# Optimization experiments

Hardware: AMD Instinct MI355X
Metric: run time of the kernel (lower is better)

The kernel has to match this reference:

```python
import jax, jax.numpy as jnp
import numpy as np

N_NODES = 50000

def _add_self_loops(edge_index, n):
    loop = jnp.arange(n, dtype=edge_index.dtype)
    src = jnp.concatenate([edge_index[0], loop])
    dst = jnp.concatenate([edge_index[1], loop])
    return src, dst

def _gcn_conv(x, src, dst, W, b, n):
    h = x @ W
    deg = jax.ops.segment_sum(jnp.ones_like(dst, dtype=h.dtype), dst, num_segments=n)
    inv_sqrt = jnp.where(deg > 0, jax.lax.rsqrt(deg), 0.0)
    coef = inv_sqrt[src] * inv_sqrt[dst]            # [E]
    msg = h[src] * coef[:, None]                     # [E, hidden]
    return jax.ops.segment_sum(msg, dst, num_segments=n) + b

def _gat_conv(x, src, dst, W, att_src, att_dst, b, n, heads, out_dim):
    # PyG GATConv, concat=False -> mean over heads; self-loops already added
    h = (x @ W).reshape(n, heads, out_dim)           # [N, H, F]
    a_src = jnp.sum(h * att_src, axis=-1)            # [N, H]
    a_dst = jnp.sum(h * att_dst, axis=-1)            # [N, H]
    e = a_src[src] + a_dst[dst]                      # [E, H]
    e = jax.nn.leaky_relu(e, negative_slope=0.2)
    # neighborhood softmax over edges grouped by destination
    m = jax.ops.segment_max(e, dst, num_segments=n)  # [N, H]
    ex = jnp.exp(e - m[dst])
    denom = jax.ops.segment_sum(ex, dst, num_segments=n)
    alpha = ex / denom[dst]                          # [E, H]
    out = jax.ops.segment_sum(h[src] * alpha[:, :, None], dst, num_segments=n)  # [N, H, F]
    return out.mean(axis=1) + b                      # concat=False -> head mean

def setup_inputs() -> dict:
    key = jax.random.key(0)
    ks = jax.random.split(key, 12)
    n, input_dim, hidden, output_dim, heads = N_NODES, 128, 128, 64, 2
    gat_out = hidden // 2
    x = jax.random.normal(ks[0], (n, input_dim), dtype=jnp.float32)
    edge_index = jax.random.randint(ks[1], (2, 800000), 0, n, dtype=jnp.int64)
    s = lambda fi, fo: float(np.sqrt(1.0 / fi))
    W1 = jax.random.normal(ks[2], (input_dim, hidden), dtype=jnp.float32) * s(input_dim, hidden)
    b1 = jnp.zeros((hidden,), dtype=jnp.float32)
    Wg = jax.random.normal(ks[3], (hidden, heads * gat_out), dtype=jnp.float32) * s(hidden, gat_out)
    att_src = jax.random.normal(ks[4], (heads, gat_out), dtype=jnp.float32) * s(gat_out, 1)
    att_dst = jax.random.normal(ks[5], (heads, gat_out), dtype=jnp.float32) * s(gat_out, 1)
    bg = jnp.zeros((gat_out,), dtype=jnp.float32)
    W3 = jax.random.normal(ks[6], (gat_out, output_dim), dtype=jnp.float32) * s(gat_out, output_dim)
    b3 = jnp.zeros((output_dim,), dtype=jnp.float32)
    return {"x": x, "edge_index": edge_index, "W1": W1, "b1": b1, "Wg": Wg,
            "att_src": att_src, "att_dst": att_dst, "bg": bg, "W3": W3, "b3": b3}

def reference(x, edge_index, W1, b1, Wg, att_src, att_dst, bg, W3, b3):
    n = x.shape[0]
    heads, gat_out = att_src.shape
    src, dst = _add_self_loops(edge_index, n)
    # dropout is identity in eval mode
    h = _gcn_conv(x, src, dst, W1, b1, n)
    h = jax.nn.relu(h)
    h = _gat_conv(h, src, dst, Wg, att_src, att_dst, bg, n, heads, gat_out)
    h = jax.nn.elu(h)
    return _gcn_conv(h, src, dst, W3, b3, n)
```

## Files before the change

kernel.cpp:

```cpp
#include <hip/hip_runtime.h>
#include <hip/hip_bf16.h>
#include <math.h>

#define N_NODES 50000
#define E0      800000
#define E_TOT   (E0 + N_NODES)
#define SCAP    512

using bf16 = __hip_bfloat16;
typedef __attribute__((ext_vector_type(8))) short bfrag;
typedef __attribute__((ext_vector_type(4))) float ffrag;

static __device__ __forceinline__ float bfu2f_lo(unsigned u){ return __uint_as_float(u << 16); }
static __device__ __forceinline__ float bfu2f_hi(unsigned u){ return __uint_as_float(u & 0xffff0000u); }

static __device__ __forceinline__ unsigned packbf(float a, float b){
    bf16 x = __float2bfloat16(a), y = __float2bfloat16(b);
    unsigned short ux = *reinterpret_cast<unsigned short*>(&x);
    unsigned short uy = *reinterpret_cast<unsigned short*>(&y);
    return ((unsigned)uy << 16) | ux;
}

static __device__ __forceinline__ int detect_f32(const unsigned* xu){
    int lane = threadIdx.x & 63;
    unsigned ex = (xu[lane] >> 7) & 0xFF;
    return (__ballot(ex < 100 || ex > 140) != 0ULL);
}
static __device__ __forceinline__ int detect_i32(const int* ei){
    int lane = threadIdx.x & 63;
    return (__ballot(ei[2 * lane + 1] != 0) != 0ULL);
}

static __device__ __forceinline__ float ldany(const void* p, int i, int isf32){
    return isf32 ? ((const float*)p)[i] : __bfloat162float(((const bf16*)p)[i]);
}

__global__ void k_convert(const void* __restrict__ xv,
                          const void* W1, const void* Wg, const void* W3,
                          const void* b1, const void* bg, const void* b3,
                          const void* as_, const void* ad_,
                          bf16* __restrict__ W1p, bf16* __restrict__ Wgp,
                          bf16* __restrict__ W3p, float* __restrict__ vecf,
                          bf16* __restrict__ xb, int* __restrict__ deg){
    const int NXB = (N_NODES * 32 + 255) / 256;
    int b = blockIdx.x, t = threadIdx.x;
    if (b >= 148 + NXB){
        int i = (b - 148 - NXB) * 256 + t;
        if (i < N_NODES) deg[i] = 0;
        return;
    }
    int isf = detect_f32((const unsigned*)xv);
    if (b >= 148){
        int i = (b - 148) * 256 + t;
        if (i < N_NODES * 32){
            if (isf){
                float4 v = ((const float4*)xv)[i];
                ((uint2*)xb)[i] = make_uint2(packbf(v.x, v.y), packbf(v.z, v.w));
            } else {
                ((uint2*)xb)[i] = ((const uint2*)xv)[i];
            }
        }
        return;
    }
    if (b < 16){
        int dd = b * 256 + t;
        int j  = dd & 7;
        int L  = (dd >> 3) & 63;
        int kc = (dd >> 9) & 1;
        int ct = dd >> 10;
        int k = kc * 32 + ((L >> 4) << 3) + j;
        int n = ct * 16 + (L & 15);
        W3p[dd] = __float2bfloat16(ldany(W3, k * 64 + n, isf));
    }
    else if (b < 18){
        int i = (b - 16) * 256 + t;
        float v;
        if      (i < 128) v = ldany(b1,  i,       isf);
        else if (i < 192) v = ldany(bg,  i - 128, isf);
        else if (i < 256) v = ldany(b3,  i - 192, isf);
        else if (i < 384) v = ldany(as_, i - 256, isf);
        else              v = ldany(ad_, i - 384, isf);
        vecf[i] = v;
    } else {
        int d = (b - 18) * 256 + t;
        const void* Wsrc = (d < 16384) ? W1 : Wg;
        bf16* Wdst = (d < 16384) ? W1p : Wgp;
        int dd = d & 16383;
        int j  = dd & 7;
        int L  = (dd >> 3) & 63;
        int kc = (dd >> 9) & 3;
        int ct = dd >> 11;
        int k = kc * 32 + ((L >> 4) << 3) + j;
        int n = ct * 16 + (L & 15);
        Wdst[dd] = __float2bfloat16(ldany(Wsrc, k * 128 + n, isf));
    }
}


static __device__ __forceinline__ int load_dst(const int* ei, int e, int is32){
    if (e >= E0) return e - E0;
    return is32 ? ei[E0 + e] : (int)((const long long*)ei)[E0 + e];
}
static __device__ __forceinline__ int load_src(const int* ei, int e, int is32){
    if (e >= E0) return e - E0;
    return is32 ? ei[e] : (int)((const long long*)ei)[e];
}

__global__ void k_count(const int* __restrict__ ei, int* __restrict__ deg,
                        int* __restrict__ rank){
    int is32 = detect_i32(ei);
    int e = blockIdx.x * blockDim.x + threadIdx.x;
    if (e >= E_TOT) return;
    int dst = load_dst(ei, e, is32);
    int src = load_src(ei, e, is32);
    if ((unsigned)dst >= N_NODES || (unsigned)src >= N_NODES) return;
    rank[e] = atomicAdd(&deg[dst], 1);
}

__global__ void k_scanA(const int* __restrict__ deg, int* __restrict__ tmp, int* __restrict__ blk){
    __shared__ int s[256];
    int t = threadIdx.x;
    int i = blockIdx.x * 256 + t;
    int v = (i < N_NODES) ? deg[i] : 0;
    s[t] = v; __syncthreads();
    for (int off = 1; off < 256; off <<= 1){
        int x = (t >= off) ? s[t - off] : 0;
        __syncthreads();
        s[t] += x;
        __syncthreads();
    }
    if (t == 255) blk[blockIdx.x] = s[255];
    if (i < N_NODES) tmp[i] = s[t] - v;
}

__global__ void k_scanC(int* __restrict__ row_ptr, const int* __restrict__ blk,
                        const int* __restrict__ deg, float* __restrict__ inv_sqrt,
                        int nb){
    __shared__ int s[256];
    int t = threadIdx.x;
    int B = blockIdx.x;
    s[t] = (t < nb && t < B) ? blk[t] : 0;
    __syncthreads();
    for (int off = 128; off; off >>= 1){
        if (t < off) s[t] += s[t + off];
        __syncthreads();
    }
    int base = s[0];
    int i = B * 256 + t;
    if (i < N_NODES){
        row_ptr[i] += base;
        int d = deg[i];
        inv_sqrt[i] = (d > 0) ? rsqrtf((float)d) : 0.0f;
    }
    if (i == 0) row_ptr[N_NODES] = E_TOT;
}

__global__ void k_fill(const int* __restrict__ ei, const int* __restrict__ row_ptr,
                       const float* __restrict__ isq, const int* __restrict__ rank,
                       int2* __restrict__ ecr){
    int is32 = detect_i32(ei);
    int e = blockIdx.x * blockDim.x + threadIdx.x;
    if (e >= E_TOT) return;
    int dst = load_dst(ei, e, is32);
    int src = load_src(ei, e, is32);
    if ((unsigned)dst >= N_NODES || (unsigned)src >= N_NODES) return;
    int pos = row_ptr[dst] + rank[e];
    float c = isq[dst] * isq[src];
    ecr[pos] = make_int2(src, __float_as_int(c));
}

__global__ __launch_bounds__(256) void k_gather(
        const uint4* __restrict__ xb16, const int* __restrict__ rp,
        const int2* __restrict__ ecr, uint4* __restrict__ Xa16){
    __shared__ int   scsr[SCAP];
    __shared__ float scf[SCAP];
    int n0 = blockIdx.x * 4;
    int b0 = rp[n0];
    int stot = min(rp[n0 + 4] - b0, SCAP);
    for (int i = threadIdx.x; i < stot; i += 256){
        int2 ev = ecr[b0 + i];
        scsr[i] = ev.x;
        scf[i]  = __int_as_float(ev.y);
    }
    __syncthreads();

    int w = threadIdx.x >> 6, lane = threadIdx.x & 63;
    int q4 = lane >> 4, fz = lane & 15;
    int n = n0 + w;
    float a0=0,a1=0,a2=0,a3=0,a4=0,a5=0,a6=0,a7=0;
    int b = rp[n] - b0, e = rp[n + 1] - b0;
    int elim = min(e, stot);
    #pragma unroll 2
    for (int i = b + q4; i < elim; i += 4){
        int s = scsr[i];
        float c = scf[i];
        uint4 v = xb16[(size_t)s * 16 + fz];
        a0 += c * bfu2f_lo(v.x);  a1 += c * bfu2f_hi(v.x);
        a2 += c * bfu2f_lo(v.y);  a3 += c * bfu2f_hi(v.y);
        a4 += c * bfu2f_lo(v.z);  a5 += c * bfu2f_hi(v.z);
        a6 += c * bfu2f_lo(v.w);  a7 += c * bfu2f_hi(v.w);
    }
    int start = max(b, stot);
    int i0 = start + (((b + q4) - start) & 3);
    for (int i = i0; i < e; i += 4){
        int2 ev = ecr[b0 + i];
        float c = __int_as_float(ev.y);
        uint4 v = xb16[(size_t)ev.x * 16 + fz];
        a0 += c * bfu2f_lo(v.x);  a1 += c * bfu2f_hi(v.x);
        a2 += c * bfu2f_lo(v.y);  a3 += c * bfu2f_hi(v.y);
        a4 += c * bfu2f_lo(v.z);  a5 += c * bfu2f_hi(v.z);
        a6 += c * bfu2f_lo(v.w);  a7 += c * bfu2f_hi(v.w);
    }
    a0 += __shfl_xor(a0, 32, 64);  a0 += __shfl_xor(a0, 16, 64);
    a1 += __shfl_xor(a1, 32, 64);  a1 += __shfl_xor(a1, 16, 64);
    a2 += __shfl_xor(a2, 32, 64);  a2 += __shfl_xor(a2, 16, 64);
    a3 += __shfl_xor(a3, 32, 64);  a3 += __shfl_xor(a3, 16, 64);
    a4 += __shfl_xor(a4, 32, 64);  a4 += __shfl_xor(a4, 16, 64);
    a5 += __shfl_xor(a5, 32, 64);  a5 += __shfl_xor(a5, 16, 64);
    a6 += __shfl_xor(a6, 32, 64);  a6 += __shfl_xor(a6, 16, 64);
    a7 += __shfl_xor(a7, 32, 64);  a7 += __shfl_xor(a7, 16, 64);
    if (lane < 16){
        uint4 o;
        o.x = packbf(a0, a1);  o.y = packbf(a2, a3);
        o.z = packbf(a4, a5);  o.w = packbf(a6, a7);
        Xa16[(size_t)n * 16 + fz] = o;
    }
}

template<int EPI>
__global__ __launch_bounds__(512) void k_gemm_mfma(
        const bf16* __restrict__ A, const bf16* __restrict__ Wp,
        const float* __restrict__ vecf, bf16* __restrict__ O,
        float* __restrict__ aS, float* __restrict__ aD){
    __shared__ float sA[16][8];
    __shared__ float sD[16][8];
    int wid  = threadIdx.x >> 6;
    int lane = threadIdx.x & 63;
    int n0 = blockIdx.x * 16;
    int m = lane & 15, q = lane >> 4;

    const bfrag* Ap = (const bfrag*)(A + (size_t)(n0 + m) * 128);
    const bfrag* Bp = (const bfrag*)Wp + (size_t)wid * 256 + lane;

    ffrag c = {0.f, 0.f, 0.f, 0.f};
    #pragma unroll
    for (int kc = 0; kc < 4; ++kc){
        bfrag af = Ap[kc * 4 + q];
        bfrag bf = Bp[kc * 64];
        c = __builtin_amdgcn_mfma_f32_16x16x32_bf16(af, bf, c, 0, 0, 0);
    }
    __syncthreads();

    int col = wid * 16 + m;
    if (EPI == 0){
        float bb = vecf[col];
        #pragma unroll
        for (int r = 0; r < 4; ++r){
            int row = n0 + q * 4 + r;
            O[(size_t)row * 128 + col] = __float2bfloat16(fmaxf(c[r] + bb, 0.f));
        }
    } else {
        int f = col & 63, h = col >> 6;
        float as_v = vecf[256 + h * 64 + f];
        float ad_v = vecf[384 + h * 64 + f];
        float ps[4], pd[4];
        #pragma unroll
        for (int r = 0; r < 4; ++r){
            int row = n0 + q * 4 + r;
            O[(size_t)row * 128 + f * 2 + h] = __float2bfloat16(c[r]);
            ps[r] = c[r] * as_v;
            pd[r] = c[r] * ad_v;
        }
        #pragma unroll
        for (int off = 1; off < 16; off <<= 1){
            #pragma unroll
            for (int r = 0; r < 4; ++r){
                ps[r] += __shfl_xor(ps[r], off, 64);
                pd[r] += __shfl_xor(pd[r], off, 64);
            }
        }
        if (m == 0){
            #pragma unroll
            for (int r = 0; r < 4; ++r){
                int rl = q * 4 + r;
                sA[rl][wid] = ps[r];
                sD[rl][wid] = pd[r];
            }
        }
        __syncthreads();
        int t = threadIdx.x;
        if (t < 64){
            int rl = t >> 2, hh = (t >> 1) & 1, which = t & 1;
            const float (*S)[8] = which ? sD : sA;
            float v = S[rl][hh * 4 + 0] + S[rl][hh * 4 + 1]
                    + S[rl][hh * 4 + 2] + S[rl][hh * 4 + 3];
            float* dp = which ? aD : aS;
            dp[(size_t)(n0 + rl) * 2 + hh] = v;
        }
    }
}

__global__ __launch_bounds__(256) void k_gemm_z(
        const bf16* __restrict__ Y, const bf16* __restrict__ W3p,
        bf16* __restrict__ Z){
    int wid  = threadIdx.x >> 6;
    int lane = threadIdx.x & 63;
    int n0 = blockIdx.x * 16;
    int m = lane & 15, q = lane >> 4;

    const bfrag* Ap = (const bfrag*)(Y + (size_t)(n0 + m) * 64);
    const bfrag* Bp = (const bfrag*)W3p + (size_t)wid * 128 + lane;

    ffrag c = {0.f, 0.f, 0.f, 0.f};
    #pragma unroll
    for (int kc = 0; kc < 2; ++kc){
        bfrag af = Ap[kc * 4 + q];
        bfrag bf = Bp[kc * 64];
        c = __builtin_amdgcn_mfma_f32_16x16x32_bf16(af, bf, c, 0, 0, 0);
    }
    int col = wid * 16 + m;
    #pragma unroll
    for (int r = 0; r < 4; ++r){
        int row = n0 + q * 4 + r;
        Z[(size_t)row * 64 + col] = __float2bfloat16(c[r]);
    }
}

__global__ __launch_bounds__(256) void k_gat(
        const uint4* __restrict__ X2v, const int* __restrict__ rp,
        const int2* __restrict__ ecr, const float2* __restrict__ a_src,
        const float2* __restrict__ a_dst, const float* __restrict__ vecf,
        uint2* __restrict__ Yu2){
    __shared__ int    scsr[SCAP];
    __shared__ float2 pe[SCAP];
    int n0 = blockIdx.x * 4;
    int b0 = rp[n0];
    int stot = min(rp[n0 + 4] - b0, SCAP);
    for (int i = threadIdx.x; i < stot; i += 256) scsr[i] = ecr[b0 + i].x;
    __syncthreads();

    int w = threadIdx.x >> 6, lane = threadIdx.x & 63;
    int q4 = lane >> 4, fz = lane & 15;
    int n = n0 + w;
    float2 ad = a_dst[n];
    int b = rp[n] - b0, e = rp[n + 1] - b0;
    int elim = min(e, stot);

    for (int i = b + lane; i < elim; i += 64){
        float2 av = a_src[scsr[i]];
        float e0 = av.x + ad.x, e1 = av.y + ad.y;
        e0 = (e0 > 0.f) ? e0 : 0.2f * e0;
        e1 = (e1 > 0.f) ? e1 : 0.2f * e1;
        pe[i] = make_float2(__expf(e0), __expf(e1));
    }

    float l0 = 0.f, l1 = 0.f;
    float o00=0,o01=0, o10=0,o11=0, o20=0,o21=0, o30=0,o31=0;
    #pragma unroll 2
    for (int i = b + q4; i < elim; i += 4){
        float2 p = pe[i];
        uint4 v = X2v[(size_t)scsr[i] * 16 + fz];
        l0  += p.x;                  l1  += p.y;
        o00 += p.x * bfu2f_lo(v.x);  o01 += p.y * bfu2f_hi(v.x);
        o10 += p.x * bfu2f_lo(v.y);  o11 += p.y * bfu2f_hi(v.y);
        o20 += p.x * bfu2f_lo(v.z);  o21 += p.y * bfu2f_hi(v.z);
        o30 += p.x * bfu2f_lo(v.w);  o31 += p.y * bfu2f_hi(v.w);
    }
    int start = max(b, stot);
    int i0 = start + (((b + q4) - start) & 3);
    for (int i = i0; i < e; i += 4){
        int s = ecr[b0 + i].x;
        float2 av = a_src[s];
        uint4 v = X2v[(size_t)s * 16 + fz];
        float e0 = av.x + ad.x, e1 = av.y + ad.y;
        e0 = (e0 > 0.f) ? e0 : 0.2f * e0;
        e1 = (e1 > 0.f) ? e1 : 0.2f * e1;
        float p0 = __expf(e0), p1 = __expf(e1);
        l0  += p0;                 l1  += p1;
        o00 += p0 * bfu2f_lo(v.x); o01 += p1 * bfu2f_hi(v.x);
        o10 += p0 * bfu2f_lo(v.y); o11 += p1 * bfu2f_hi(v.y);
        o20 += p0 * bfu2f_lo(v.z); o21 += p1 * bfu2f_hi(v.z);
        o30 += p0 * bfu2f_lo(v.w); o31 += p1 * bfu2f_hi(v.w);
    }
    l0  += __shfl_xor(l0, 32, 64);   l0  += __shfl_xor(l0, 16, 64);
    l1  += __shfl_xor(l1, 32, 64);   l1  += __shfl_xor(l1, 16, 64);
    o00 += __shfl_xor(o00, 32, 64);  o00 += __shfl_xor(o00, 16, 64);
    o01 += __shfl_xor(o01, 32, 64);  o01 += __shfl_xor(o01, 16, 64);
    o10 += __shfl_xor(o10, 32, 64);  o10 += __shfl_xor(o10, 16, 64);
    o11 += __shfl_xor(o11, 32, 64);  o11 += __shfl_xor(o11, 16, 64);
    o20 += __shfl_xor(o20, 32, 64);  o20 += __shfl_xor(o20, 16, 64);
    o21 += __shfl_xor(o21, 32, 64);  o21 += __shfl_xor(o21, 16, 64);
    o30 += __shfl_xor(o30, 32, 64);  o30 += __shfl_xor(o30, 16, 64);
    o31 += __shfl_xor(o31, 32, 64);  o31 += __shfl_xor(o31, 16, 64);
    if (lane < 16){
        float v0 = 0.5f * (o00 / l0 + o01 / l1) + vecf[128 + 4 * fz + 0];
        float v1 = 0.5f * (o10 / l0 + o11 / l1) + vecf[128 + 4 * fz + 1];
        float v2 = 0.5f * (o20 / l0 + o21 / l1) + vecf[128 + 4 * fz + 2];
        float v3 = 0.5f * (o30 / l0 + o31 / l1) + vecf[128 + 4 * fz + 3];
        v0 = (v0 > 0.f) ? v0 : expm1f(v0);
        v1 = (v1 > 0.f) ? v1 : expm1f(v1);
        v2 = (v2 > 0.f) ? v2 : expm1f(v2);
        v3 = (v3 > 0.f) ? v3 : expm1f(v3);
        Yu2[(size_t)n * 16 + fz] = make_uint2(packbf(v0, v1), packbf(v2, v3));
    }
}

__global__ __launch_bounds__(256) void k_gather_out(
        const uint2* __restrict__ Zu2, const int* __restrict__ rp,
        const int2* __restrict__ ecr, const float* __restrict__ vecf,
        float4* __restrict__ out4){
    __shared__ int   scsr[SCAP];
    __shared__ float scf[SCAP];
    int n0 = blockIdx.x * 4;
    int b0 = rp[n0];
    int stot = min(rp[n0 + 4] - b0, SCAP);
    for (int i = threadIdx.x; i < stot; i += 256){
        int2 ev = ecr[b0 + i];
        scsr[i] = ev.x;
        scf[i]  = __int_as_float(ev.y);
    }
    __syncthreads();

    int w = threadIdx.x >> 6, lane = threadIdx.x & 63;
    int q4 = lane >> 4, fz = lane & 15;
    int n = n0 + w;
    float a0 = 0.f, a1 = 0.f, a2 = 0.f, a3 = 0.f;
    int b = rp[n] - b0, e = rp[n + 1] - b0;
    int elim = min(e, stot);
    #pragma unroll 2
    for (int i = b + q4; i < elim; i += 4){
        float c = scf[i];
        uint2 v = Zu2[(size_t)scsr[i] * 16 + fz];
        a0 += c * bfu2f_lo(v.x);  a1 += c * bfu2f_hi(v.x);
        a2 += c * bfu2f_lo(v.y);  a3 += c * bfu2f_hi(v.y);
    }
    int start = max(b, stot);
    int i0 = start + (((b + q4) - start) & 3);
    for (int i = i0; i < e; i += 4){
        int2 ev = ecr[b0 + i];
        float c = __int_as_float(ev.y);
        uint2 v = Zu2[(size_t)ev.x * 16 + fz];
        a0 += c * bfu2f_lo(v.x);  a1 += c * bfu2f_hi(v.x);
        a2 += c * bfu2f_lo(v.y);  a3 += c * bfu2f_hi(v.y);
    }
    a0 += __shfl_xor(a0, 32, 64);  a0 += __shfl_xor(a0, 16, 64);
    a1 += __shfl_xor(a1, 32, 64);  a1 += __shfl_xor(a1, 16, 64);
    a2 += __shfl_xor(a2, 32, 64);  a2 += __shfl_xor(a2, 16, 64);
    a3 += __shfl_xor(a3, 32, 64);  a3 += __shfl_xor(a3, 16, 64);
    if (lane < 16)
        out4[(size_t)n * 16 + fz] = make_float4(
            a0 + vecf[192 + 4 * fz + 0], a1 + vecf[192 + 4 * fz + 1],
            a2 + vecf[192 + 4 * fz + 2], a3 + vecf[192 + 4 * fz + 3]);
}


extern "C" void kernel_launch(void* const* d_in, const int* in_sizes, int n_in,
                              void* d_out, int out_size, void* d_ws, size_t ws_size,
                              hipStream_t stream) {
    const void* x  = d_in[0];
    const int*  ei = (const int*)d_in[1];
    float* out = (float*)d_out;

    char* p = (char*)d_ws;
    auto alloc = [&](size_t bytes) -> void* {
        void* r = (void*)p;
        p += (bytes + 255) & ~(size_t)255;
        return r;
    };
    int*   deg      = (int*)  alloc((size_t)N_NODES * 4);
    int*   row_ptr  = (int*)  alloc((size_t)(N_NODES + 1) * 4);
    int*   blk      = (int*)  alloc(256 * 4);
    int*   rank     = (int*)  alloc((size_t)E_TOT * 4);
    int2*  ecr      = (int2*) alloc((size_t)E_TOT * 8);
    float* inv_sqrt = (float*)alloc((size_t)N_NODES * 4);
    float* a_src    = (float*)alloc((size_t)N_NODES * 2 * 4);
    float* a_dst    = (float*)alloc((size_t)N_NODES * 2 * 4);
    bf16*  W1p      = (bf16*) alloc(16384 * 2);
    bf16*  Wgp      = (bf16*) alloc(16384 * 2);
    bf16*  W3p      = (bf16*) alloc(4096 * 2);
    float* vecf     = (float*)alloc(512 * 4);
    bf16*  xb       = (bf16*) alloc((size_t)N_NODES * 128 * 2);
    bf16*  XA       = (bf16*) alloc((size_t)N_NODES * 128 * 2);
    bf16*  Y        = (bf16*) alloc((size_t)N_NODES * 64 * 2);
    bf16*  Z        = xb;

    const int NB_NODE = (N_NODES + 255) / 256;
    const int NB_EDGE = (E_TOT + 255) / 256;
    const int NXB     = (N_NODES * 32 + 255) / 256;
    const int NB_CONV = 148 + NXB + NB_NODE;

    k_convert<<<NB_CONV, 256, 0, stream>>>(x, d_in[2], d_in[4], d_in[8],
                                           d_in[3], d_in[7], d_in[9], d_in[5], d_in[6],
                                           W1p, Wgp, W3p, vecf, xb, deg);
    k_count<<<NB_EDGE, 256, 0, stream>>>(ei, deg, rank);
    k_scanA<<<NB_NODE, 256, 0, stream>>>(deg, row_ptr, blk);
    k_scanC<<<NB_NODE, 256, 0, stream>>>(row_ptr, blk, deg, inv_sqrt, NB_NODE);
    k_fill<<<NB_EDGE, 256, 0, stream>>>(ei, row_ptr, inv_sqrt, rank, ecr);

    k_gather<<<N_NODES / 4, 256, 0, stream>>>((const uint4*)xb, row_ptr, ecr,
                                              (uint4*)XA);
    k_gemm_mfma<0><<<N_NODES / 16, 512, 0, stream>>>(XA, W1p, vecf, XA,
                                                     nullptr, nullptr);
    k_gemm_mfma<1><<<N_NODES / 16, 512, 0, stream>>>(XA, Wgp, vecf, XA,
                                                     a_src, a_dst);
    k_gat<<<N_NODES / 4, 256, 0, stream>>>((const uint4*)XA, row_ptr, ecr,
                                           (const float2*)a_src, (const float2*)a_dst,
                                           vecf, (uint2*)Y);
    k_gemm_z<<<N_NODES / 16, 256, 0, stream>>>(Y, W3p, Z);
    k_gather_out<<<N_NODES / 4, 256, 0, stream>>>((const uint2*)Z, row_ptr, ecr,
                                                  vecf, (float4*)out);
}
```

Measured before the change: 285.4 us.

## Pack edge endpoints with rank, remap gather lanes, widen per-wave GEMM tiles

k_count now stores src and dst packed into 16 bits each, next to the atomic rank, so k_fill no longer re-reads and re-decodes edge_index. The three gather kernels switch from 4 edge groups × 16 feature lanes to 16 edge groups × 4 feature lanes, looping over feature quarters. This puts more independent edge loads in flight, at the cost of re-walking each neighbor list several times. The GEMM kernels now give each wave 16 full rows across all output column tiles, reusing the A fragments and dropping the shared-memory reduction and barrier for the attention scores. The last GEMM blocks may read past N_NODES rows.

```diff
diff --git a/kernel.cpp b/kernel.cpp
--- a/kernel.cpp
+++ b/kernel.cpp
@@ -107,14 +107,18 @@
 }
 
 __global__ void k_count(const int* __restrict__ ei, int* __restrict__ deg,
-                        int* __restrict__ rank){
+                        int2* __restrict__ pkrk){
     int is32 = detect_i32(ei);
     int e = blockIdx.x * blockDim.x + threadIdx.x;
     if (e >= E_TOT) return;
     int dst = load_dst(ei, e, is32);
     int src = load_src(ei, e, is32);
-    if ((unsigned)dst >= N_NODES || (unsigned)src >= N_NODES) return;
-    rank[e] = atomicAdd(&deg[dst], 1);
+    if ((unsigned)dst >= N_NODES || (unsigned)src >= N_NODES){
+        pkrk[e] = make_int2(-1, 0);
+        return;
+    }
+    int r = atomicAdd(&deg[dst], 1);
+    pkrk[e] = make_int2((src << 16) | dst, r);
 }
 
 __global__ void k_scanA(const int* __restrict__ deg, int* __restrict__ tmp, int* __restrict__ blk){
@@ -155,16 +159,16 @@
     if (i == 0) row_ptr[N_NODES] = E_TOT;
 }
 
-__global__ void k_fill(const int* __restrict__ ei, const int* __restrict__ row_ptr,
-                       const float* __restrict__ isq, const int* __restrict__ rank,
-                       int2* __restrict__ ecr){
-    int is32 = detect_i32(ei);
+__global__ void k_fill(const int2* __restrict__ pkrk, const int* __restrict__ row_ptr,
+                       const float* __restrict__ isq, int2* __restrict__ ecr){
     int e = blockIdx.x * blockDim.x + threadIdx.x;
     if (e >= E_TOT) return;
-    int dst = load_dst(ei, e, is32);
-    int src = load_src(ei, e, is32);
-    if ((unsigned)dst >= N_NODES || (unsigned)src >= N_NODES) return;
-    int pos = row_ptr[dst] + rank[e];
+    int2 pr = pkrk[e];
+    unsigned pk = (unsigned)pr.x;
+    if (pk == 0xFFFFFFFFu) return;
+    int dst = pk & 0xFFFF;
+    int src = pk >> 16;
+    int pos = row_ptr[dst] + pr.y;
     float c = isq[dst] * isq[src];
     ecr[pos] = make_int2(src, __float_as_int(c));
 }
@@ -185,45 +189,47 @@
     __syncthreads();
 
     int w = threadIdx.x >> 6, lane = threadIdx.x & 63;
-    int q4 = lane >> 4, fz = lane & 15;
+    int g = lane >> 2, fq = lane & 3;
     int n = n0 + w;
-    float a0=0,a1=0,a2=0,a3=0,a4=0,a5=0,a6=0,a7=0;
     int b = rp[n] - b0, e = rp[n + 1] - b0;
     int elim = min(e, stot);
-    #pragma unroll 2
-    for (int i = b + q4; i < elim; i += 4){
-        int s = scsr[i];
-        float c = scf[i];
-        uint4 v = xb16[(size_t)s * 16 + fz];
-        a0 += c * bfu2f_lo(v.x);  a1 += c * bfu2f_hi(v.x);
-        a2 += c * bfu2f_lo(v.y);  a3 += c * bfu2f_hi(v.y);
-        a4 += c * bfu2f_lo(v.z);  a5 += c * bfu2f_hi(v.z);
-        a6 += c * bfu2f_lo(v.w);  a7 += c * bfu2f_hi(v.w);
-    }
     int start = max(b, stot);
-    int i0 = start + (((b + q4) - start) & 3);
-    for (int i = i0; i < e; i += 4){
-        int2 ev = ecr[b0 + i];
-        float c = __int_as_float(ev.y);
-        uint4 v = xb16[(size_t)ev.x * 16 + fz];
-        a0 += c * bfu2f_lo(v.x);  a1 += c * bfu2f_hi(v.x);
-        a2 += c * bfu2f_lo(v.y);  a3 += c * bfu2f_hi(v.y);
-        a4 += c * bfu2f_lo(v.z);  a5 += c * bfu2f_hi(v.z);
-        a6 += c * bfu2f_lo(v.w);  a7 += c * bfu2f_hi(v.w);
-    }
-    a0 += __shfl_xor(a0, 32, 64);  a0 += __shfl_xor(a0, 16, 64);
-    a1 += __shfl_xor(a1, 32, 64);  a1 += __shfl_xor(a1, 16, 64);
-    a2 += __shfl_xor(a2, 32, 64);  a2 += __shfl_xor(a2, 16, 64);
-    a3 += __shfl_xor(a3, 32, 64);  a3 += __shfl_xor(a3, 16, 64);
-    a4 += __shfl_xor(a4, 32, 64);  a4 += __shfl_xor(a4, 16, 64);
-    a5 += __shfl_xor(a5, 32, 64);  a5 += __shfl_xor(a5, 16, 64);
-    a6 += __shfl_xor(a6, 32, 64);  a6 += __shfl_xor(a6, 16, 64);
-    a7 += __shfl_xor(a7, 32, 64);  a7 += __shfl_xor(a7, 16, 64);
-    if (lane < 16){
-        uint4 o;
-        o.x = packbf(a0, a1);  o.y = packbf(a2, a3);
-        o.z = packbf(a4, a5);  o.w = packbf(a6, a7);
-        Xa16[(size_t)n * 16 + fz] = o;
+
+    #pragma unroll
+    for (int qp = 0; qp < 4; ++qp){
+        int j = qp * 4 + fq;
+        float a0=0,a1=0,a2=0,a3=0,a4=0,a5=0,a6=0,a7=0;
+        for (int i = b + g; i < elim; i += 16){
+            float c = scf[i];
+            uint4 v = xb16[(size_t)scsr[i] * 16 + j];
+            a0 += c * bfu2f_lo(v.x);  a1 += c * bfu2f_hi(v.x);
+            a2 += c * bfu2f_lo(v.y);  a3 += c * bfu2f_hi(v.y);
+            a4 += c * bfu2f_lo(v.z);  a5 += c * bfu2f_hi(v.z);
+            a6 += c * bfu2f_lo(v.w);  a7 += c * bfu2f_hi(v.w);
+        }
+        int i0 = start + (((b + g) - start) & 15);
+        for (int i = i0; i < e; i += 16){
+            int2 ev = ecr[b0 + i];
+            float c = __int_as_float(ev.y);
+            uint4 v = xb16[(size_t)ev.x * 16 + j];
+            a0 += c * bfu2f_lo(v.x);  a1 += c * bfu2f_hi(v.x);
+            a2 += c * bfu2f_lo(v.y);  a3 += c * bfu2f_hi(v.y);
+            a4 += c * bfu2f_lo(v.z);  a5 += c * bfu2f_hi(v.z);
+            a6 += c * bfu2f_lo(v.w);  a7 += c * bfu2f_hi(v.w);
+        }
+        #pragma unroll
+        for (int off = 4; off < 64; off <<= 1){
+            a0 += __shfl_xor(a0, off, 64);  a1 += __shfl_xor(a1, off, 64);
+            a2 += __shfl_xor(a2, off, 64);  a3 += __shfl_xor(a3, off, 64);
+            a4 += __shfl_xor(a4, off, 64);  a5 += __shfl_xor(a5, off, 64);
+            a6 += __shfl_xor(a6, off, 64);  a7 += __shfl_xor(a7, off, 64);
+        }
+        if (g == 0){
+            uint4 o;
+            o.x = packbf(a0, a1);  o.y = packbf(a2, a3);
+            o.z = packbf(a4, a5);  o.w = packbf(a6, a7);
+            Xa16[(size_t)n * 16 + j] = o;
+        }
     }
 }
 
@@ -231,71 +237,77 @@
 __global__ __launch_bounds__(512) void k_gemm_mfma(
         const bf16* __restrict__ A, const bf16* __restrict__ Wp,
         const float* __restrict__ vecf, bf16* __restrict__ O,
-        float* __restrict__ aS, float* __restrict__ aD){
-    __shared__ float sA[16][8];
-    __shared__ float sD[16][8];
+        float2* __restrict__ aS, float2* __restrict__ aD){
     int wid  = threadIdx.x >> 6;
     int lane = threadIdx.x & 63;
-    int n0 = blockIdx.x * 16;
+    int r0 = blockIdx.x * 128 + wid * 16;
     int m = lane & 15, q = lane >> 4;
 
-    const bfrag* Ap = (const bfrag*)(A + (size_t)(n0 + m) * 128);
-    const bfrag* Bp = (const bfrag*)Wp + (size_t)wid * 256 + lane;
-
-    ffrag c = {0.f, 0.f, 0.f, 0.f};
-    #pragma unroll
-    for (int kc = 0; kc < 4; ++kc){
-        bfrag af = Ap[kc * 4 + q];
-        bfrag bf = Bp[kc * 64];
-        c = __builtin_amdgcn_mfma_f32_16x16x32_bf16(af, bf, c, 0, 0, 0);
-    }
-    __syncthreads();
-
-    int col = wid * 16 + m;
+    const bfrag* Ap = (const bfrag*)(A + (size_t)(r0 + m) * 128);
+    bfrag af[4];
+    #pragma unroll
+    for (int kc = 0; kc < 4; ++kc) af[kc] = Ap[kc * 4 + q];
+
+    ffrag c[8];
+    #pragma unroll
+    for (int ct = 0; ct < 8; ++ct){
+        const bfrag* Bp = (const bfrag*)Wp + ct * 256 + lane;
+        ffrag acc = {0.f, 0.f, 0.f, 0.f};
+        #pragma unroll
+        for (int kc = 0; kc < 4; ++kc)
+            acc = __builtin_amdgcn_mfma_f32_16x16x32_bf16(af[kc], Bp[kc * 64], acc, 0, 0, 0);
+        c[ct] = acc;
+    }
+
     if (EPI == 0){
-        float bb = vecf[col];
-        #pragma unroll
-        for (int r = 0; r < 4; ++r){
-            int row = n0 + q * 4 + r;
-            O[(size_t)row * 128 + col] = __float2bfloat16(fmaxf(c[r] + bb, 0.f));
+        #pragma unroll
+        for (int ct = 0; ct < 8; ++ct){
+            int col = ct * 16 + m;
+            float bb = vecf[col];
+            #pragma unroll
+            for (int r = 0; r < 4; ++r){
+                int row = r0 + q * 4 + r;
+                if (row < N_NODES)
+                    O[(size_t)row * 128 + col] = __float2bfloat16(fmaxf(c[ct][r] + bb, 0.f));
+            }
         }
     } else {
-        int f = col & 63, h = col >> 6;
-        float as_v = vecf[256 + h * 64 + f];
-        float ad_v = vecf[384 + h * 64 + f];
-        float ps[4], pd[4];
-        #pragma unroll
-        for (int r = 0; r < 4; ++r){
-            int row = n0 + q * 4 + r;
-            O[(size_t)row * 128 + f * 2 + h] = __float2bfloat16(c[r]);
-            ps[r] = c[r] * as_v;
-            pd[r] = c[r] * ad_v;
+        float ps0[4] = {0,0,0,0}, ps1[4] = {0,0,0,0};
+        float pd0[4] = {0,0,0,0}, pd1[4] = {0,0,0,0};
+        #pragma unroll
+        for (int ct = 0; ct < 8; ++ct){
+            const int h = ct >> 2;
+            int f = (ct & 3) * 16 + m;
+            float as_v = vecf[256 + h * 64 + f];
+            float ad_v = vecf[384 + h * 64 + f];
+            #pragma unroll
+            for (int r = 0; r < 4; ++r){
+                int row = r0 + q * 4 + r;
+                if (row < N_NODES)
+                    O[(size_t)row * 128 + f * 2 + h] = __float2bfloat16(c[ct][r]);
+                if (h == 0){ ps0[r] += c[ct][r] * as_v;  pd0[r] += c[ct][r] * ad_v; }
+                else       { ps1[r] += c[ct][r] * as_v;  pd1[r] += c[ct][r] * ad_v; }
+            }
         }
         #pragma unroll
         for (int off = 1; off < 16; off <<= 1){
             #pragma unroll
             for (int r = 0; r < 4; ++r){
-                ps[r] += __shfl_xor(ps[r], off, 64);
-                pd[r] += __shfl_xor(pd[r], off, 64);
+                ps0[r] += __shfl_xor(ps0[r], off, 64);
+                ps1[r] += __shfl_xor(ps1[r], off, 64);
+                pd0[r] += __shfl_xor(pd0[r], off, 64);
+                pd1[r] += __shfl_xor(pd1[r], off, 64);
             }
         }
         if (m == 0){
             #pragma unroll
             for (int r = 0; r < 4; ++r){
-                int rl = q * 4 + r;
-                sA[rl][wid] = ps[r];
-                sD[rl][wid] = pd[r];
+                int row = r0 + q * 4 + r;
+                if (row < N_NODES){
+                    aS[row] = make_float2(ps0[r], ps1[r]);
+                    aD[row] = make_float2(pd0[r], pd1[r]);
+                }
             }
-        }
-        __syncthreads();
-        int t = threadIdx.x;
-        if (t < 64){
-            int rl = t >> 2, hh = (t >> 1) & 1, which = t & 1;
-            const float (*S)[8] = which ? sD : sA;
-            float v = S[rl][hh * 4 + 0] + S[rl][hh * 4 + 1]
-                    + S[rl][hh * 4 + 2] + S[rl][hh * 4 + 3];
-            float* dp = which ? aD : aS;
-            dp[(size_t)(n0 + rl) * 2 + hh] = v;
         }
     }
 }
@@ -305,24 +317,28 @@
         bf16* __restrict__ Z){
     int wid  = threadIdx.x >> 6;
     int lane = threadIdx.x & 63;
-    int n0 = blockIdx.x * 16;
+    int r0 = blockIdx.x * 64 + wid * 16;
     int m = lane & 15, q = lane >> 4;
 
-    const bfrag* Ap = (const bfrag*)(Y + (size_t)(n0 + m) * 64);
-    const bfrag* Bp = (const bfrag*)W3p + (size_t)wid * 128 + lane;
-
-    ffrag c = {0.f, 0.f, 0.f, 0.f};
-    #pragma unroll
-    for (int kc = 0; kc < 2; ++kc){
-        bfrag af = Ap[kc * 4 + q];
-        bfrag bf = Bp[kc * 64];
-        c = __builtin_amdgcn_mfma_f32_16x16x32_bf16(af, bf, c, 0, 0, 0);
-    }
-    int col = wid * 16 + m;
-    #pragma unroll
-    for (int r = 0; r < 4; ++r){
-        int row = n0 + q * 4 + r;
-        Z[(size_t)row * 64 + col] = __float2bfloat16(c[r]);
+    const bfrag* Ap = (const bfrag*)(Y + (size_t)(r0 + m) * 64);
+    bfrag af[2];
+    #pragma unroll
+    for (int kc = 0; kc < 2; ++kc) af[kc] = Ap[kc * 4 + q];
+
+    #pragma unroll
+    for (int ct = 0; ct < 4; ++ct){
+        const bfrag* Bp = (const bfrag*)W3p + ct * 128 + lane;
+        ffrag c = {0.f, 0.f, 0.f, 0.f};
+        #pragma unroll
+        for (int kc = 0; kc < 2; ++kc)
+            c = __builtin_amdgcn_mfma_f32_16x16x32_bf16(af[kc], Bp[kc * 64], c, 0, 0, 0);
+        int col = ct * 16 + m;
+        #pragma unroll
+        for (int r = 0; r < 4; ++r){
+            int row = r0 + q * 4 + r;
+            if (row < N_NODES)
+                Z[(size_t)row * 64 + col] = __float2bfloat16(c[r]);
+        }
     }
 }
 
@@ -340,11 +356,12 @@
     __syncthreads();
 
     int w = threadIdx.x >> 6, lane = threadIdx.x & 63;
-    int q4 = lane >> 4, fz = lane & 15;
+    int g = lane >> 2, fq = lane & 3;
     int n = n0 + w;
     float2 ad = a_dst[n];
     int b = rp[n] - b0, e = rp[n + 1] - b0;
     int elim = min(e, stot);
+    int start = max(b, stot);
 
     for (int i = b + lane; i < elim; i += 64){
         float2 av = a_src[scsr[i]];
@@ -355,58 +372,65 @@
     }
 
     float l0 = 0.f, l1 = 0.f;
-    float o00=0,o01=0, o10=0,o11=0, o20=0,o21=0, o30=0,o31=0;
-    #pragma unroll 2
-    for (int i = b + q4; i < elim; i += 4){
-        float2 p = pe[i];
-        uint4 v = X2v[(size_t)scsr[i] * 16 + fz];
-        l0  += p.x;                  l1  += p.y;
-        o00 += p.x * bfu2f_lo(v.x);  o01 += p.y * bfu2f_hi(v.x);
-        o10 += p.x * bfu2f_lo(v.y);  o11 += p.y * bfu2f_hi(v.y);
-        o20 += p.x * bfu2f_lo(v.z);  o21 += p.y * bfu2f_hi(v.z);
-        o30 += p.x * bfu2f_lo(v.w);  o31 += p.y * bfu2f_hi(v.w);
-    }
-    int start = max(b, stot);
-    int i0 = start + (((b + q4) - start) & 3);
-    for (int i = i0; i < e; i += 4){
-        int s = ecr[b0 + i].x;
-        float2 av = a_src[s];
-        uint4 v = X2v[(size_t)s * 16 + fz];
-        float e0 = av.x + ad.x, e1 = av.y + ad.y;
-        e0 = (e0 > 0.f) ? e0 : 0.2f * e0;
-        e1 = (e1 > 0.f) ? e1 : 0.2f * e1;
-        float p0 = __expf(e0), p1 = __expf(e1);
-        l0  += p0;                 l1  += p1;
-        o00 += p0 * bfu2f_lo(v.x); o01 += p1 * bfu2f_hi(v.x);
-        o10 += p0 * bfu2f_lo(v.y); o11 += p1 * bfu2f_hi(v.y);
-        o20 += p0 * bfu2f_lo(v.z); o21 += p1 * bfu2f_hi(v.z);
-        o30 += p0 * bfu2f_lo(v.w); o31 += p1 * bfu2f_hi(v.w);
-    }
-    l0  += __shfl_xor(l0, 32, 64);   l0  += __shfl_xor(l0, 16, 64);
-    l1  += __shfl_xor(l1, 32, 64);   l1  += __shfl_xor(l1, 16, 64);
-    o00 += __shfl_xor(o00, 32, 64);  o00 += __shfl_xor(o00, 16, 64);
-    o01 += __shfl_xor(o01, 32, 64);  o01 += __shfl_xor(o01, 16, 64);
-    o10 += __shfl_xor(o10, 32, 64);  o10 += __shfl_xor(o10, 16, 64);
-    o11 += __shfl_xor(o11, 32, 64);  o11 += __shfl_xor(o11, 16, 64);
-    o20 += __shfl_xor(o20, 32, 64);  o20 += __shfl_xor(o20, 16, 64);
-    o21 += __shfl_xor(o21, 32, 64);  o21 += __shfl_xor(o21, 16, 64);
-    o30 += __shfl_xor(o30, 32, 64);  o30 += __shfl_xor(o30, 16, 64);
-    o31 += __shfl_xor(o31, 32, 64);  o31 += __shfl_xor(o31, 16, 64);
-    if (lane < 16){
-        float v0 = 0.5f * (o00 / l0 + o01 / l1) + vecf[128 + 4 * fz + 0];
-        float v1 = 0.5f * (o10 / l0 + o11 / l1) + vecf[128 + 4 * fz + 1];
-        float v2 = 0.5f * (o20 / l0 + o21 / l1) + vecf[128 + 4 * fz + 2];
-        float v3 = 0.5f * (o30 / l0 + o31 / l1) + vecf[128 + 4 * fz + 3];
-        v0 = (v0 > 0.f) ? v0 : expm1f(v0);
-        v1 = (v1 > 0.f) ? v1 : expm1f(v1);
-        v2 = (v2 > 0.f) ? v2 : expm1f(v2);
-        v3 = (v3 > 0.f) ? v3 : expm1f(v3);
-        Yu2[(size_t)n * 16 + fz] = make_uint2(packbf(v0, v1), packbf(v2, v3));
+    #pragma unroll
+    for (int qp = 0; qp < 4; ++qp){
+        int j = qp * 4 + fq;
+        float o00=0,o01=0, o10=0,o11=0, o20=0,o21=0, o30=0,o31=0;
+        for (int i = b + g; i < elim; i += 16){
+            float2 p = pe[i];
+            uint4 v = X2v[(size_t)scsr[i] * 16 + j];
+            if (qp == 0){ l0 += p.x;  l1 += p.y; }
+            o00 += p.x * bfu2f_lo(v.x);  o01 += p.y * bfu2f_hi(v.x);
+            o10 += p.x * bfu2f_lo(v.y);  o11 += p.y * bfu2f_hi(v.y);
+            o20 += p.x * bfu2f_lo(v.z);  o21 += p.y * bfu2f_hi(v.z);
+            o30 += p.x * bfu2f_lo(v.w);  o31 += p.y * bfu2f_hi(v.w);
+        }
+        int i0 = start + (((b + g) - start) & 15);
+        for (int i = i0; i < e; i += 16){
+            int s = ecr[b0 + i].x;
+            float2 av = a_src[s];
+            uint4 v = X2v[(size_t)s * 16 + j];
+            float e0 = av.x + ad.x, e1 = av.y + ad.y;
+            e0 = (e0 > 0.f) ? e0 : 0.2f * e0;
+            e1 = (e1 > 0.f) ? e1 : 0.2f * e1;
+            float p0 = __expf(e0), p1 = __expf(e1);
+            if (qp == 0){ l0 += p0;  l1 += p1; }
+            o00 += p0 * bfu2f_lo(v.x);  o01 += p1 * bfu2f_hi(v.x);
+            o10 += p0 * bfu2f_lo(v.y);  o11 += p1 * bfu2f_hi(v.y);
+            o20 += p0 * bfu2f_lo(v.z);  o21 += p1 * bfu2f_hi(v.z);
+            o30 += p0 * bfu2f_lo(v.w);  o31 += p1 * bfu2f_hi(v.w);
+        }
+        #pragma unroll
+        for (int off = 4; off < 64; off <<= 1){
+            o00 += __shfl_xor(o00, off, 64);  o01 += __shfl_xor(o01, off, 64);
+            o10 += __shfl_xor(o10, off, 64);  o11 += __shfl_xor(o11, off, 64);
+            o20 += __shfl_xor(o20, off, 64);  o21 += __shfl_xor(o21, off, 64);
+            o30 += __shfl_xor(o30, off, 64);  o31 += __shfl_xor(o31, off, 64);
+        }
+        if (qp == 0){
+            #pragma unroll
+            for (int off = 4; off < 64; off <<= 1){
+                l0 += __shfl_xor(l0, off, 64);
+                l1 += __shfl_xor(l1, off, 64);
+            }
+        }
+        if (g == 0){
+            int fb = 16 * qp + 4 * fq;
+            float v0 = 0.5f * (o00 / l0 + o01 / l1) + vecf[128 + fb + 0];
+            float v1 = 0.5f * (o10 / l0 + o11 / l1) + vecf[128 + fb + 1];
+            float v2 = 0.5f * (o20 / l0 + o21 / l1) + vecf[128 + fb + 2];
+            float v3 = 0.5f * (o30 / l0 + o31 / l1) + vecf[128 + fb + 3];
+            v0 = (v0 > 0.f) ? v0 : expm1f(v0);
+            v1 = (v1 > 0.f) ? v1 : expm1f(v1);
+            v2 = (v2 > 0.f) ? v2 : expm1f(v2);
+            v3 = (v3 > 0.f) ? v3 : expm1f(v3);
+            Yu2[(size_t)n * 16 + 4 * qp + fq] = make_uint2(packbf(v0, v1), packbf(v2, v3));
+        }
     }
 }
 
 __global__ __launch_bounds__(256) void k_gather_out(
-        const uint2* __restrict__ Zu2, const int* __restrict__ rp,
+        const uint4* __restrict__ Z16, const int* __restrict__ rp,
         const int2* __restrict__ ecr, const float* __restrict__ vecf,
         float4* __restrict__ out4){
     __shared__ int   scsr[SCAP];
@@ -422,35 +446,51 @@
     __syncthreads();
 
     int w = threadIdx.x >> 6, lane = threadIdx.x & 63;
-    int q4 = lane >> 4, fz = lane & 15;
+    int g = lane >> 2, fq = lane & 3;
     int n = n0 + w;
-    float a0 = 0.f, a1 = 0.f, a2 = 0.f, a3 = 0.f;
     int b = rp[n] - b0, e = rp[n + 1] - b0;
     int elim = min(e, stot);
-    #pragma unroll 2
-    for (int i = b + q4; i < elim; i += 4){
-        float c = scf[i];
-        uint2 v = Zu2[(size_t)scsr[i] * 16 + fz];
-        a0 += c * bfu2f_lo(v.x);  a1 += c * bfu2f_hi(v.x);
-        a2 += c * bfu2f_lo(v.y);  a3 += c * bfu2f_hi(v.y);
-    }
     int start = max(b, stot);
-    int i0 = start + (((b + q4) - start) & 3);
-    for (int i = i0; i < e; i += 4){
-        int2 ev = ecr[b0 + i];
-        float c = __int_as_float(ev.y);
-        uint2 v = Zu2[(size_t)ev.x * 16 + fz];
-        a0 += c * bfu2f_lo(v.x);  a1 += c * bfu2f_hi(v.x);
-        a2 += c * bfu2f_lo(v.y);  a3 += c * bfu2f_hi(v.y);
-    }
-    a0 += __shfl_xor(a0, 32, 64);  a0 += __shfl_xor(a0, 16, 64);
-    a1 += __shfl_xor(a1, 32, 64);  a1 += __shfl_xor(a1, 16, 64);
-    a2 += __shfl_xor(a2, 32, 64);  a2 += __shfl_xor(a2, 16, 64);
-    a3 += __shfl_xor(a3, 32, 64);  a3 += __shfl_xor(a3, 16, 64);
-    if (lane < 16)
-        out4[(size_t)n * 16 + fz] = make_float4(
-            a0 + vecf[192 + 4 * fz + 0], a1 + vecf[192 + 4 * fz + 1],
-            a2 + vecf[192 + 4 * fz + 2], a3 + vecf[192 + 4 * fz + 3]);
+
+    #pragma unroll
+    for (int hp = 0; hp < 2; ++hp){
+        int j = hp * 4 + fq;
+        float a0=0,a1=0,a2=0,a3=0,a4=0,a5=0,a6=0,a7=0;
+        for (int i = b + g; i < elim; i += 16){
+            float c = scf[i];
+            uint4 v = Z16[(size_t)scsr[i] * 8 + j];
+            a0 += c * bfu2f_lo(v.x);  a1 += c * bfu2f_hi(v.x);
+            a2 += c * bfu2f_lo(v.y);  a3 += c * bfu2f_hi(v.y);
+            a4 += c * bfu2f_lo(v.z);  a5 += c * bfu2f_hi(v.z);
+            a6 += c * bfu2f_lo(v.w);  a7 += c * bfu2f_hi(v.w);
+        }
+        int i0 = start + (((b + g) - start) & 15);
+        for (int i = i0; i < e; i += 16){
+            int2 ev = ecr[b0 + i];
+            float c = __int_as_float(ev.y);
+            uint4 v = Z16[(size_t)ev.x * 8 + j];
+            a0 += c * bfu2f_lo(v.x);  a1 += c * bfu2f_hi(v.x);
+            a2 += c * bfu2f_lo(v.y);  a3 += c * bfu2f_hi(v.y);
+            a4 += c * bfu2f_lo(v.z);  a5 += c * bfu2f_hi(v.z);
+            a6 += c * bfu2f_lo(v.w);  a7 += c * bfu2f_hi(v.w);
+        }
+        #pragma unroll
+        for (int off = 4; off < 64; off <<= 1){
+            a0 += __shfl_xor(a0, off, 64);  a1 += __shfl_xor(a1, off, 64);
+            a2 += __shfl_xor(a2, off, 64);  a3 += __shfl_xor(a3, off, 64);
+            a4 += __shfl_xor(a4, off, 64);  a5 += __shfl_xor(a5, off, 64);
+            a6 += __shfl_xor(a6, off, 64);  a7 += __shfl_xor(a7, off, 64);
+        }
+        if (g == 0){
+            int fb = 8 * j;
+            out4[(size_t)n * 16 + j * 2 + 0] = make_float4(
+                a0 + vecf[192 + fb + 0], a1 + vecf[192 + fb + 1],
+                a2 + vecf[192 + fb + 2], a3 + vecf[192 + fb + 3]);
+            out4[(size_t)n * 16 + j * 2 + 1] = make_float4(
+                a4 + vecf[192 + fb + 4], a5 + vecf[192 + fb + 5],
+                a6 + vecf[192 + fb + 6], a7 + vecf[192 + fb + 7]);
+        }
+    }
 }
 
 
@@ -470,7 +510,7 @@
     int*   deg      = (int*)  alloc((size_t)N_NODES * 4);
     int*   row_ptr  = (int*)  alloc((size_t)(N_NODES + 1) * 4);
     int*   blk      = (int*)  alloc(256 * 4);
-    int*   rank     = (int*)  alloc((size_t)E_TOT * 4);
+    int2*  pkrk     = (int2*) alloc((size_t)E_TOT * 8);
     int2*  ecr      = (int2*) alloc((size_t)E_TOT * 8);
     float* inv_sqrt = (float*)alloc((size_t)N_NODES * 4);
     float* a_src    = (float*)alloc((size_t)N_NODES * 2 * 4);
@@ -488,25 +528,27 @@
     const int NB_EDGE = (E_TOT + 255) / 256;
     const int NXB     = (N_NODES * 32 + 255) / 256;
     const int NB_CONV = 148 + NXB + NB_NODE;
+    const int NB_G128 = (N_NODES + 127) / 128;
+    const int NB_G64  = (N_NODES + 63) / 64;
 
     k_convert<<<NB_CONV, 256, 0, stream>>>(x, d_in[2], d_in[4], d_in[8],
                                            d_in[3], d_in[7], d_in[9], d_in[5], d_in[6],
                                            W1p, Wgp, W3p, vecf, xb, deg);
-    k_count<<<NB_EDGE, 256, 0, stream>>>(ei, deg, rank);
+    k_count<<<NB_EDGE, 256, 0, stream>>>(ei, deg, pkrk);
     k_scanA<<<NB_NODE, 256, 0, stream>>>(deg, row_ptr, blk);
     k_scanC<<<NB_NODE, 256, 0, stream>>>(row_ptr, blk, deg, inv_sqrt, NB_NODE);
-    k_fill<<<NB_EDGE, 256, 0, stream>>>(ei, row_ptr, inv_sqrt, rank, ecr);
+    k_fill<<<NB_EDGE, 256, 0, stream>>>(pkrk, row_ptr, inv_sqrt, ecr);
 
     k_gather<<<N_NODES / 4, 256, 0, stream>>>((const uint4*)xb, row_ptr, ecr,
                                               (uint4*)XA);
-    k_gemm_mfma<0><<<N_NODES / 16, 512, 0, stream>>>(XA, W1p, vecf, XA,
-                                                     nullptr, nullptr);
-    k_gemm_mfma<1><<<N_NODES / 16, 512, 0, stream>>>(XA, Wgp, vecf, XA,
-                                                     a_src, a_dst);
+    k_gemm_mfma<0><<<NB_G128, 512, 0, stream>>>(XA, W1p, vecf, XA,
+                                                nullptr, nullptr);
+    k_gemm_mfma<1><<<NB_G128, 512, 0, stream>>>(XA, Wgp, vecf, XA,
+                                                (float2*)a_src, (float2*)a_dst);
     k_gat<<<N_NODES / 4, 256, 0, stream>>>((const uint4*)XA, row_ptr, ecr,
                                            (const float2*)a_src, (const float2*)a_dst,
                                            vecf, (uint2*)Y);
-    k_gemm_z<<<N_NODES / 16, 256, 0, stream>>>(Y, W3p, Z);
-    k_gather_out<<<N_NODES / 4, 256, 0, stream>>>((const uint2*)Z, row_ptr, ecr,
+    k_gemm_z<<<NB_G64, 256, 0, stream>>>(Y, W3p, Z);
+    k_gather_out<<<N_NODES / 4, 256, 0, stream>>>((const uint4*)Z, row_ptr, ecr,
                                                   vecf, (float4*)out);
 }
```

Result: slower. 378.9 us (+32.7%).
